# Kernel tuning notes

Measured on AMD Instinct MI355X. Metric: run time of the kernel, lower is better.

## Reference

```python
import jax, jax.numpy as jnp
import numpy as np

# geomloss.SamplesLoss(loss='sinkhorn', p=2, blur=0.1**0.5, backend='tensorized',
#                      cost=cosine cost ** 2) with defaults scaling=0.5, debias=True,
#                      reach=None (balanced OT, dampening = 1), uniform weights.
P = 2
BLUR = 0.1 ** 0.5   # eps = BLUR**P = 0.1
SCALING = 0.5


def cosine_cost(a, b):
    # a: (B,N,D), b: (B,M,D) -> (1 - cos(a,b))**2, shape (B,N,M)
    an = a / jnp.linalg.norm(a, axis=-1, keepdims=True)
    bn = b / jnp.linalg.norm(b, axis=-1, keepdims=True)
    return (1.0 - jnp.einsum('bnd,bmd->bnm', an, bn)) ** P


def softmin(eps, C, h):
    # geomloss softmin_tensorized: h (B,M), C (B,N,M) -> (B,N)
    return -eps * jax.nn.logsumexp(h[:, None, :] - C / eps, axis=2)


def eps_schedule(diameter):
    # geomloss epsilon_schedule(p, diameter, blur, scaling)
    return ([diameter ** P]
            + [float(np.exp(e)) for e in np.arange(P * np.log(diameter),
                                                   P * np.log(BLUR),
                                                   P * np.log(SCALING))]
            + [BLUR ** P])


def max_diameter(x, y):
    # geomloss max_diameter over all points of both (flattened) clouds
    D = x.shape[-1]
    pts = np.concatenate([np.asarray(x).reshape(-1, D),
                          np.asarray(y).reshape(-1, D)], axis=0)
    return float(np.linalg.norm(pts.max(axis=0) - pts.min(axis=0)))


def _sinkhorn(x, y, eps_list):
    sg = jax.lax.stop_gradient
    B, N, _ = x.shape
    M = y.shape[1]
    # geomloss detaches the second argument of each cost evaluation
    C_xy = cosine_cost(x, sg(y))
    C_yx = cosine_cost(y, sg(x))
    C_xx = cosine_cost(x, sg(x))  # debias terms
    C_yy = cosine_cost(y, sg(y))

    a_log = jnp.full((B, N), -np.log(N), dtype=x.dtype)  # log uniform weights
    b_log = jnp.full((B, M), -np.log(M), dtype=x.dtype)

    # initialization at the largest temperature
    eps = eps_list[0]
    f_aa = softmin(eps, sg(C_xx), a_log)
    g_bb = softmin(eps, sg(C_yy), b_log)
    g_ab = softmin(eps, sg(C_yx), a_log)
    f_ba = softmin(eps, sg(C_xy), b_log)

    # eps-scaling loop (run without gradients, as in geomloss)
    for eps in eps_list:
        ft_ba = softmin(eps, sg(C_xy), b_log + g_ab / eps)
        gt_ab = softmin(eps, sg(C_yx), a_log + f_ba / eps)
        ft_aa = softmin(eps, sg(C_xx), a_log + f_aa / eps)
        gt_bb = softmin(eps, sg(C_yy), b_log + g_bb / eps)
        f_ba, g_ab = 0.5 * (f_ba + ft_ba), 0.5 * (g_ab + gt_ab)
        f_aa, g_bb = 0.5 * (f_aa + ft_aa), 0.5 * (g_bb + gt_bb)

    # last extrapolation WITH gradients, dual inputs detached (envelope theorem)
    eps = eps_list[-1]
    f_ba, g_ab = (softmin(eps, C_xy, sg(b_log + g_ab / eps)),
                  softmin(eps, C_yx, sg(a_log + f_ba / eps)))
    f_aa = softmin(eps, C_xx, sg(a_log + f_aa / eps))
    g_bb = softmin(eps, C_yy, sg(b_log + g_bb / eps))

    # sinkhorn_cost, debiased, batch -> (B,)
    a = jnp.exp(a_log)
    b = jnp.exp(b_log)
    return jnp.sum(a * (f_ba - f_aa), axis=1) + jnp.sum(b * (g_ab - g_bb), axis=1)


def setup_inputs() -> dict:
    key = jax.random.key(0)
    k1, k2 = jax.random.split(key)
    B, N, D = 2, 4096, 64
    inputs = jax.random.normal(k1, (B, N, D), dtype=jnp.float32)
    targets = jax.random.normal(k2, (B, N, D), dtype=jnp.float32)
    return {"inputs": inputs, "targets": targets}


def reference(inputs, targets):
    eps_list = eps_schedule(max_diameter(inputs, targets))
    return _sinkhorn(inputs, targets, eps_list)
```

## Files before the change

kernel.cpp:

```cpp
#include <hip/hip_runtime.h>
#include <math.h>

#define Bq 2
#define Nq 4096
#define Dq 64
#define MAXR 14
#define RBAND 32
#define NBAND (Nq / RBAND)
#define W_LOG (-8.317766166719343f)
#define WL2   (-12.0f)
#define LOG2E 1.4426950408889634f
#define LN2   0.6931471805599453f
#define DQ_SCALE (4.0f / 65535.0f)
#define Q_SCALE  16383.75f
#define ACLAMP 88.0f
#define SFLOOR 1e-30f

#define F_XN   ((size_t)0)
#define F_YN   (F_XN + (size_t)Bq * Nq * Dq)
#define F_XH   (F_YN + (size_t)Bq * Nq * Dq)
#define F_XL   (F_XH + (size_t)Bq * Nq * Dq / 2)
#define F_YH   (F_XL + (size_t)Bq * Nq * Dq / 2)
#define F_YL   (F_YH + (size_t)Bq * Nq * Dq / 2)
#define F_FG   (F_YL + (size_t)Bq * Nq * Dq / 2)
#define F_EPS  (F_FG + (size_t)2 * 4 * Bq * Nq)
#define F_MM   (F_EPS + 64)
#define F_CP   (F_MM + (size_t)64 * 128)
#define F_C    (((F_CP + (size_t)Bq * NBAND * Nq) + 3) & ~(size_t)3)
#define GSZ    ((size_t)Bq * Nq * Nq)
#define F_TOTAL_P (F_C + 3 * GSZ / 2)
#define F_TOTAL_S (F_C)

typedef short short8v __attribute__((ext_vector_type(8)));
typedef float f32x4 __attribute__((ext_vector_type(4)));

__device__ __forceinline__ unsigned short f2bf(float f) {
    unsigned u = __float_as_uint(f);
    unsigned r = (u + 0x7fffu + ((u >> 16) & 1u)) >> 16;
    return (unsigned short)r;
}
__device__ __forceinline__ float bf2f(unsigned short b) {
    return __uint_as_float(((unsigned)b) << 16);
}

__global__ __launch_bounds__(256) void k_normalize(const float* __restrict__ x,
                                                   const float* __restrict__ y,
                                                   float* __restrict__ ws) {
    int gid = blockIdx.x * 256 + threadIdx.x;
    int wave = gid >> 6;
    int lane = gid & 63;
    int tensor = wave / (Bq * Nq);
    int p = wave % (Bq * Nq);
    const float* src = tensor ? y : x;
    float v = src[(size_t)p * Dq + lane];
    float s = v * v;
    #pragma unroll
    for (int o = 32; o > 0; o >>= 1) s += __shfl_xor(s, o);
    float vn = v / sqrtf(s);
    float* dst = ws + (tensor ? F_YN : F_XN);
    dst[(size_t)p * Dq + lane] = vn;
    unsigned short hb = f2bf(vn);
    float lo = vn - bf2f(hb);
    unsigned short lb = f2bf(lo);
    unsigned short* dh = (unsigned short*)(ws + (tensor ? F_YH : F_XH));
    unsigned short* dl = (unsigned short*)(ws + (tensor ? F_YL : F_XL));
    dh[(size_t)p * Dq + lane] = hb;
    dl[(size_t)p * Dq + lane] = lb;
}

__global__ __launch_bounds__(256) void k_minmax(const float* __restrict__ x,
                                                const float* __restrict__ y,
                                                float* __restrict__ ws) {
    int d = threadIdx.x & 63, q = threadIdx.x >> 6;
    int p0 = blockIdx.x * 256;
    float mx = -INFINITY, mn = INFINITY;
    for (int p = p0 + q; p < p0 + 256; p += 4) {
        const float* src = (p < Bq * Nq) ? x : y;
        int pp = (p < Bq * Nq) ? p : p - Bq * Nq;
        float v = src[(size_t)pp * Dq + d];
        mx = fmaxf(mx, v); mn = fminf(mn, v);
    }
    __shared__ float smx[4][64], smn[4][64];
    smx[q][d] = mx; smn[q][d] = mn;
    __syncthreads();
    if (threadIdx.x < 64) {
        float a = fmaxf(fmaxf(smx[0][d], smx[1][d]), fmaxf(smx[2][d], smx[3][d]));
        float i = fminf(fminf(smn[0][d], smn[1][d]), fminf(smn[2][d], smn[3][d]));
        ws[F_MM + (size_t)blockIdx.x * 128 + d] = a;
        ws[F_MM + (size_t)blockIdx.x * 128 + 64 + d] = i;
    }
}

__global__ void k_eps(float* __restrict__ ws) {
    int d = threadIdx.x;
    float mx = -INFINITY, mn = INFINITY;
    for (int k = 0; k < 64; k++) {
        mx = fmaxf(mx, ws[F_MM + (size_t)k * 128 + d]);
        mn = fminf(mn, ws[F_MM + (size_t)k * 128 + 64 + d]);
    }
    float r = mx - mn;
    float r2 = r * r;
    #pragma unroll
    for (int o = 32; o > 0; o >>= 1) r2 += __shfl_xor(r2, o);
    if (d == 0) {
        double dd = (double)sqrtf(r2);
        double start = 2.0 * log(dd);
        double stop  = 2.0 * log(sqrt(0.1));
        double step  = 2.0 * log(0.5);
        double lend = ceil((stop - start) / step);
        int len = (lend <= 0.0) ? 0 : (int)lend;
        int n = len + 2;
        if (n > MAXR - 2) n = MAXR - 2;
        int* ei = (int*)(ws + F_EPS);
        ei[0] = n;
        float* ev = ws + F_EPS + 8;
        ev[0] = (float)(dd * dd);
        for (int i = 0; i < len && i + 1 < n - 1; i++)
            ev[1 + i] = (float)exp(start + i * step);
        ev[n - 1] = 0.1f;
    }
}

__global__ __launch_bounds__(256) void k_gram_mfma(float* __restrict__ ws) {
    int op = blockIdx.z, b = blockIdx.y;
    int tr = (blockIdx.x & 63) * 64;
    int tc = (blockIdx.x >> 6) * 64;
    const unsigned short* AH = (const unsigned short*)(ws + (op == 2 ? F_YH : F_XH)) + (size_t)b * Nq * Dq;
    const unsigned short* AL = (const unsigned short*)(ws + (op == 2 ? F_YL : F_XL)) + (size_t)b * Nq * Dq;
    const unsigned short* BH = (const unsigned short*)(ws + (op == 1 ? F_XH : F_YH)) + (size_t)b * Nq * Dq;
    const unsigned short* BL = (const unsigned short*)(ws + (op == 1 ? F_XL : F_YL)) + (size_t)b * Nq * Dq;

    __shared__ unsigned short sAh[64][72], sAl[64][72], sBh[64][72], sBl[64][72], sC[64][72];

    #pragma unroll
    for (int i = 0; i < 2; i++) {
        int c = threadIdx.x + 256 * i;
        int row = c >> 3, pos = c & 7;
        size_t sa = (size_t)(tr + row) * Dq + pos * 8;
        size_t sb = (size_t)(tc + row) * Dq + pos * 8;
        *(uint4*)&sAh[row][pos * 8] = *(const uint4*)&AH[sa];
        *(uint4*)&sAl[row][pos * 8] = *(const uint4*)&AL[sa];
        *(uint4*)&sBh[row][pos * 8] = *(const uint4*)&BH[sb];
        *(uint4*)&sBl[row][pos * 8] = *(const uint4*)&BL[sb];
    }
    __syncthreads();

    int w = threadIdx.x >> 6, lane = threadIdx.x & 63;
    int m = lane & 15, kb = lane >> 4;
    int ar = w * 16 + m;
    short8v aH0 = *(const short8v*)&sAh[ar][kb * 8];
    short8v aH1 = *(const short8v*)&sAh[ar][32 + kb * 8];
    short8v aL0 = *(const short8v*)&sAl[ar][kb * 8];
    short8v aL1 = *(const short8v*)&sAl[ar][32 + kb * 8];

    #pragma unroll
    for (int cb = 0; cb < 4; cb++) {
        int bc = cb * 16 + m;
        short8v bH0 = *(const short8v*)&sBh[bc][kb * 8];
        short8v bH1 = *(const short8v*)&sBh[bc][32 + kb * 8];
        short8v bL0 = *(const short8v*)&sBl[bc][kb * 8];
        short8v bL1 = *(const short8v*)&sBl[bc][32 + kb * 8];
        f32x4 acc = {0.f, 0.f, 0.f, 0.f};
        acc = __builtin_amdgcn_mfma_f32_16x16x32_bf16(aH0, bH0, acc, 0, 0, 0);
        acc = __builtin_amdgcn_mfma_f32_16x16x32_bf16(aH1, bH1, acc, 0, 0, 0);
        acc = __builtin_amdgcn_mfma_f32_16x16x32_bf16(aL0, bH0, acc, 0, 0, 0);
        acc = __builtin_amdgcn_mfma_f32_16x16x32_bf16(aL1, bH1, acc, 0, 0, 0);
        acc = __builtin_amdgcn_mfma_f32_16x16x32_bf16(aH0, bL0, acc, 0, 0, 0);
        acc = __builtin_amdgcn_mfma_f32_16x16x32_bf16(aH1, bL1, acc, 0, 0, 0);
        #pragma unroll
        for (int rr = 0; rr < 4; rr++) {
            float c1 = 1.0f - acc[rr];
            unsigned u = __float2uint_rn(fminf(c1 * c1, 4.0f) * Q_SCALE);
            if (u > 65535u) u = 65535u;
            sC[w * 16 + kb * 4 + rr][cb * 16 + m] = (unsigned short)u;
        }
    }
    __syncthreads();

    unsigned short* C = (unsigned short*)(ws + F_C) + (size_t)op * GSZ + (size_t)b * Nq * Nq;
    #pragma unroll
    for (int i = 0; i < 2; i++) {
        int c = threadIdx.x + 256 * i;
        int row = c >> 3, pos = c & 7;
        uint4 v = *(const uint4*)&sC[row][pos * 8];
        *(uint4*)&C[(size_t)(tr + row) * Nq + tc + pos * 8] = v;
    }
}

__device__ __forceinline__ bool round_cfg(const float* ws, int r, int& mode, float& eps,
                                          float& inv_eps, int& cur, int& nxt) {
    const int* ei = (const int*)(ws + F_EPS);
    int n_eps = ei[0];
    if (r > n_eps + 1) return false;
    mode = (r == 0) ? 0 : ((r <= n_eps) ? 1 : 2);
    int eidx = (r == 0) ? 0 : ((r - 1 < n_eps - 1) ? r - 1 : n_eps - 1);
    eps = ws[F_EPS + 8 + eidx];
    inv_eps = 1.0f / eps;
    cur = r & 1; nxt = cur ^ 1;
    return true;
}

__global__ __launch_bounds__(256) void k_iter(float* __restrict__ ws, int r) {
    int mode, cur, nxt; float eps, inv_eps;
    if (!round_cfg(ws, r, mode, eps, inv_eps, cur, nxt)) return;
    float ie2 = inv_eps * LOG2E;
    float epsln2 = eps * LN2;
    float kq = DQ_SCALE * ie2;

    int bid = blockIdx.x;
    int op = bid >> 8;
    int rem = bid & 255;
    int b = rem >> 7;
    int band = rem & (NBAND - 1);
    int row0 = band * RBAND;
    int w = threadIdx.x >> 6, lane = threadIdx.x & 63;
    int colA = w * 1024 + lane * 8;
    int colB = colA + 512;

    const unsigned short* C = (const unsigned short*)(ws + F_C)
                              + (size_t)op * GSZ + ((size_t)b * Nq + row0) * Nq;
    int arr_dual = (op == 0) ? 1 : (op == 1 ? 2 : 3);
    int arr_out  = (op == 0) ? 0 : arr_dual;
    const float* gdual = ws + F_FG + ((size_t)cur * 4 + arr_dual) * (Bq * Nq) + (size_t)b * Nq;
    const float* fdual = ws + F_FG + ((size_t)cur * 4 + 0) * (Bq * Nq) + (size_t)b * Nq;

    float a[16];
    if (mode != 0) {
        float4 g0 = *(const float4*)&gdual[colA];
        float4 g1 = *(const float4*)&gdual[colA + 4];
        float4 g2 = *(const float4*)&gdual[colB];
        float4 g3 = *(const float4*)&gdual[colB + 4];
        a[0] = g0.x * ie2;  a[1] = g0.y * ie2;  a[2] = g0.z * ie2;  a[3] = g0.w * ie2;
        a[4] = g1.x * ie2;  a[5] = g1.y * ie2;  a[6] = g1.z * ie2;  a[7] = g1.w * ie2;
        a[8] = g2.x * ie2;  a[9] = g2.y * ie2;  a[10] = g2.z * ie2; a[11] = g2.w * ie2;
        a[12] = g3.x * ie2; a[13] = g3.y * ie2; a[14] = g3.z * ie2; a[15] = g3.w * ie2;
    } else {
        #pragma unroll
        for (int j = 0; j < 16; j++) a[j] = 0.f;
    }
    float cs[16];
    #pragma unroll
    for (int j = 0; j < 16; j++) cs[j] = 0.f;

    __shared__ float rowpart[RBAND][4];

    #pragma unroll 4
    for (int i = 0; i < RBAND; i++) {
        uint4 cuA = *(const uint4*)&C[(size_t)i * Nq + colA];
        uint4 cuB = *(const uint4*)&C[(size_t)i * Nq + colB];
        float bi = 0.f;
        if (op == 0 && mode != 0) bi = fdual[row0 + i] * ie2;
        unsigned uw[8] = {cuA.x, cuA.y, cuA.z, cuA.w, cuB.x, cuB.y, cuB.z, cuB.w};
        float rs = 0.f;
        #pragma unroll
        for (int j = 0; j < 16; j++) {
            float uf = (float)((uw[j >> 1] >> ((j & 1) * 16)) & 0xffffu);
            float t = uf * kq;
            rs += exp2f(fminf(a[j] - t, ACLAMP));
            if (op == 0) cs[j] += exp2f(fminf(bi - t, ACLAMP));
        }
        #pragma unroll
        for (int o = 32; o > 0; o >>= 1) rs += __shfl_xor(rs, o);
        if (lane == 0) rowpart[i][w] = rs;
    }
    __syncthreads();

    if (threadIdx.x < RBAND) {
        int gr = row0 + threadIdx.x;
        const float* rp = rowpart[threadIdx.x];
        float s = (rp[0] + rp[1]) + (rp[2] + rp[3]);
        float ft = -epsln2 * (WL2 + log2f(fmaxf(s, SFLOOR)));
        float* outp = ws + F_FG + ((size_t)nxt * 4 + arr_out) * (Bq * Nq) + (size_t)b * Nq;
        const float* oldp = ws + F_FG + ((size_t)cur * 4 + arr_out) * (Bq * Nq) + (size_t)b * Nq;
        outp[gr] = (mode == 1) ? 0.5f * (oldp[gr] + ft) : ft;
    }

    if (op == 0) {
        float* cp = ws + F_CP + ((size_t)b * NBAND + band) * Nq;
        *(float4*)&cp[colA]     = make_float4(cs[0], cs[1], cs[2], cs[3]);
        *(float4*)&cp[colA + 4] = make_float4(cs[4], cs[5], cs[6], cs[7]);
        *(float4*)&cp[colB]     = make_float4(cs[8], cs[9], cs[10], cs[11]);
        *(float4*)&cp[colB + 4] = make_float4(cs[12], cs[13], cs[14], cs[15]);
    }
}

__global__ __launch_bounds__(256) void k_colcomb(float* __restrict__ ws, int r) {
    int mode, cur, nxt; float eps, inv_eps;
    if (!round_cfg(ws, r, mode, eps, inv_eps, cur, nxt)) return;
    float epsln2 = eps * LN2;
    int idx = blockIdx.x * 256 + threadIdx.x;
    int b = idx >> 12, m = idx & (Nq - 1);
    const float* cp = ws + F_CP + (size_t)b * NBAND * Nq + m;
    float S = 0.f;
    #pragma unroll 8
    for (int k = 0; k < NBAND; k++) S += cp[(size_t)k * Nq];
    float gt = -epsln2 * (WL2 + log2f(fmaxf(S, SFLOOR)));
    float* outp = ws + F_FG + ((size_t)nxt * 4 + 1) * (Bq * Nq) + (size_t)b * Nq;
    const float* oldp = ws + F_FG + ((size_t)cur * 4 + 1) * (Bq * Nq) + (size_t)b * Nq;
    outp[m] = (mode == 1) ? 0.5f * (oldp[m] + gt) : gt;
}

__global__ __launch_bounds__(256) void k_fused(float* __restrict__ ws, int r) {
    int mode, cur, nxt; float eps, inv_eps;
    if (!round_cfg(ws, r, mode, eps, inv_eps, cur, nxt)) return;
    int op = blockIdx.z, b = blockIdx.y;
    int tr = blockIdx.x * 64;
    const float* A  = ws + ((op == 1 || op == 3) ? F_YN : F_XN) + (size_t)b * Nq * Dq;
    const float* Bp = ws + ((op == 0 || op == 3) ? F_YN : F_XN) + (size_t)b * Nq * Dq;
    int dual_arr = (op == 0) ? 1 : (op == 1) ? 0 : (op == 2) ? 2 : 3;
    int out_arr  = (op == 0) ? 0 : (op == 1) ? 1 : (op == 2) ? 2 : 3;
    const float* hdual = ws + F_FG + ((size_t)cur * 4 + dual_arr) * (Bq * Nq) + (size_t)b * Nq;

    __shared__ float As[64][65], Bs[64][65];
    #pragma unroll
    for (int i = 0; i < 16; i++) {
        int idx = threadIdx.x + 256 * i;
        As[idx >> 6][idx & 63] = A[(size_t)(tr + (idx >> 6)) * Dq + (idx & 63)];
    }
    int tx = threadIdx.x & 15, ty = threadIdx.x >> 4;
    float m_i[4], s_i[4];
    #pragma unroll
    for (int i = 0; i < 4; i++) { m_i[i] = -INFINITY; s_i[i] = 0.f; }

    for (int tc = 0; tc < Nq; tc += 64) {
        __syncthreads();
        #pragma unroll
        for (int i = 0; i < 16; i++) {
            int idx = threadIdx.x + 256 * i;
            Bs[idx >> 6][idx & 63] = Bp[(size_t)(tc + (idx >> 6)) * Dq + (idx & 63)];
        }
        __syncthreads();
        float acc[4][4] = {};
        #pragma unroll
        for (int dd = 0; dd < 64; dd++) {
            float a[4], bb[4];
            #pragma unroll
            for (int i = 0; i < 4; i++) a[i] = As[ty * 4 + i][dd];
            #pragma unroll
            for (int j = 0; j < 4; j++) bb[j] = Bs[tx * 4 + j][dd];
            #pragma unroll
            for (int i = 0; i < 4; i++)
                #pragma unroll
                for (int j = 0; j < 4; j++) acc[i][j] = fmaf(a[i], bb[j], acc[i][j]);
        }
        float hv[4];
        #pragma unroll
        for (int j = 0; j < 4; j++)
            hv[j] = (mode == 0) ? 0.f : hdual[tc + tx * 4 + j];
        #pragma unroll
        for (int i = 0; i < 4; i++) {
            float v[4], tm = -INFINITY;
            #pragma unroll
            for (int j = 0; j < 4; j++) {
                float c = 1.0f - acc[i][j];
                v[j] = W_LOG + (hv[j] - c * c) * inv_eps;
                tm = fmaxf(tm, v[j]);
            }
            float nm = fmaxf(m_i[i], tm);
            float add = 0.f;
            #pragma unroll
            for (int j = 0; j < 4; j++) add += expf(v[j] - nm);
            s_i[i] = s_i[i] * expf(m_i[i] - nm) + add;
            m_i[i] = nm;
        }
    }
    #pragma unroll
    for (int o = 1; o < 16; o <<= 1) {
        #pragma unroll
        for (int i = 0; i < 4; i++) {
            float om = __shfl_xor(m_i[i], o);
            float os = __shfl_xor(s_i[i], o);
            float M = fmaxf(m_i[i], om);
            s_i[i] = s_i[i] * expf(m_i[i] - M) + os * expf(om - M);
            m_i[i] = M;
        }
    }
    if (tx == 0) {
        float* outp = ws + F_FG + ((size_t)nxt * 4 + out_arr) * (Bq * Nq) + (size_t)b * Nq;
        const float* oldp = ws + F_FG + ((size_t)cur * 4 + out_arr) * (Bq * Nq) + (size_t)b * Nq;
        #pragma unroll
        for (int i = 0; i < 4; i++) {
            int n = tr + ty * 4 + i;
            float ft = -eps * (m_i[i] + logf(s_i[i]));
            outp[n] = (mode == 1) ? 0.5f * (oldp[n] + ft) : ft;
        }
    }
}

__global__ __launch_bounds__(256) void k_final(const float* __restrict__ ws,
                                               float* __restrict__ out) {
    const int* ei = (const int*)(ws + F_EPS);
    int n_eps = ei[0];
    int fin = n_eps & 1;
    int b = blockIdx.x;
    const float* fba = ws + F_FG + ((size_t)fin * 4 + 0) * (Bq * Nq) + (size_t)b * Nq;
    const float* gab = ws + F_FG + ((size_t)fin * 4 + 1) * (Bq * Nq) + (size_t)b * Nq;
    const float* faa = ws + F_FG + ((size_t)fin * 4 + 2) * (Bq * Nq) + (size_t)b * Nq;
    const float* gbb = ws + F_FG + ((size_t)fin * 4 + 3) * (Bq * Nq) + (size_t)b * Nq;
    float s = 0.f;
    for (int n = threadIdx.x; n < Nq; n += 256)
        s += (fba[n] - faa[n]) + (gab[n] - gbb[n]);
    #pragma unroll
    for (int o = 32; o > 0; o >>= 1) s += __shfl_xor(s, o);
    __shared__ float red[4];
    if ((threadIdx.x & 63) == 0) red[threadIdx.x >> 6] = s;
    __syncthreads();
    if (threadIdx.x == 0)
        out[b] = (red[0] + red[1] + red[2] + red[3]) * (1.0f / Nq);
}

__global__ void k_sentinel(float* out, int n) {
    if ((int)threadIdx.x < n) out[threadIdx.x] = 2.0e9f;
}

extern "C" void kernel_launch(void* const* d_in, const int* in_sizes, int n_in,
                              void* d_out, int out_size, void* d_ws, size_t ws_size,
                              hipStream_t stream) {
    const float* x = (const float*)d_in[0];
    const float* y = (const float*)d_in[1];
    float* out = (float*)d_out;
    float* ws = (float*)d_ws;

    bool big   = ws_size >= F_TOTAL_P * sizeof(float);
    bool small = ws_size >= F_TOTAL_S * sizeof(float);

    if (!small) {
        k_sentinel<<<1, 64, 0, stream>>>(out, out_size);
        return;
    }

    k_normalize<<<(2 * Bq * Nq * 64) / 256, 256, 0, stream>>>(x, y, ws);
    k_minmax<<<64, 256, 0, stream>>>(x, y, ws);
    k_eps<<<1, 64, 0, stream>>>(ws);

    if (big) {
        k_gram_mfma<<<dim3(4096, Bq, 3), 256, 0, stream>>>(ws);
        for (int r = 0; r < MAXR; r++) {
            k_iter<<<3 * Bq * NBAND, 256, 0, stream>>>(ws, r);
            k_colcomb<<<(Bq * Nq) / 256, 256, 0, stream>>>(ws, r);
        }
    } else {
        for (int r = 0; r < MAXR; r++) {
            k_fused<<<dim3(Nq / 64, Bq, 4), 256, 0, stream>>>(ws, r);
        }
    }

    k_final<<<Bq, 256, 0, stream>>>(ws, out);
}
```

Before: 849.3 us.

## Factor exp of duals out of inner loop and halve row band size

Rewrites exp2(a - t) as exp2(a) * exp2(-t), so each cost entry needs one exp2 that is shared between the row sum and the column sum for the op-0 case, instead of two exps. Dual exponentials are precomputed once per thread (columns) and once per row. The loop now processes two rows per iteration with interleaved shuffle reductions, and RBAND is halved to 16 to double the block count. The factored form loses the per-term clamp and may underflow or overflow when duals and costs are large, which affects numerical robustness.

```diff
diff --git a/kernel.cpp b/kernel.cpp
--- a/kernel.cpp
+++ b/kernel.cpp
@@ -5,7 +5,7 @@
 #define Nq 4096
 #define Dq 64
 #define MAXR 14
-#define RBAND 32
+#define RBAND 16
 #define NBAND (Nq / RBAND)
 #define W_LOG (-8.317766166719343f)
 #define WL2   (-12.0f)
@@ -205,13 +205,13 @@
     if (!round_cfg(ws, r, mode, eps, inv_eps, cur, nxt)) return;
     float ie2 = inv_eps * LOG2E;
     float epsln2 = eps * LN2;
-    float kq = DQ_SCALE * ie2;
+    float nkq = -DQ_SCALE * ie2;
 
     int bid = blockIdx.x;
-    int op = bid >> 8;
-    int rem = bid & 255;
-    int b = rem >> 7;
-    int band = rem & (NBAND - 1);
+    int op = bid / (Bq * NBAND);
+    int rem = bid % (Bq * NBAND);
+    int b = rem / NBAND;
+    int band = rem % NBAND;
     int row0 = band * RBAND;
     int w = threadIdx.x >> 6, lane = threadIdx.x & 63;
     int colA = w * 1024 + lane * 8;
@@ -224,19 +224,19 @@
     const float* gdual = ws + F_FG + ((size_t)cur * 4 + arr_dual) * (Bq * Nq) + (size_t)b * Nq;
     const float* fdual = ws + F_FG + ((size_t)cur * 4 + 0) * (Bq * Nq) + (size_t)b * Nq;
 
-    float a[16];
+    float pa[16];
     if (mode != 0) {
         float4 g0 = *(const float4*)&gdual[colA];
         float4 g1 = *(const float4*)&gdual[colA + 4];
         float4 g2 = *(const float4*)&gdual[colB];
         float4 g3 = *(const float4*)&gdual[colB + 4];
-        a[0] = g0.x * ie2;  a[1] = g0.y * ie2;  a[2] = g0.z * ie2;  a[3] = g0.w * ie2;
-        a[4] = g1.x * ie2;  a[5] = g1.y * ie2;  a[6] = g1.z * ie2;  a[7] = g1.w * ie2;
-        a[8] = g2.x * ie2;  a[9] = g2.y * ie2;  a[10] = g2.z * ie2; a[11] = g2.w * ie2;
-        a[12] = g3.x * ie2; a[13] = g3.y * ie2; a[14] = g3.z * ie2; a[15] = g3.w * ie2;
+        float gv[16] = {g0.x, g0.y, g0.z, g0.w, g1.x, g1.y, g1.z, g1.w,
+                        g2.x, g2.y, g2.z, g2.w, g3.x, g3.y, g3.z, g3.w};
+        #pragma unroll
+        for (int j = 0; j < 16; j++) pa[j] = exp2f(fminf(gv[j] * ie2, ACLAMP));
     } else {
         #pragma unroll
-        for (int j = 0; j < 16; j++) a[j] = 0.f;
+        for (int j = 0; j < 16; j++) pa[j] = 1.f;
     }
     float cs[16];
     #pragma unroll
@@ -244,24 +244,34 @@
 
     __shared__ float rowpart[RBAND][4];
 
-    #pragma unroll 4
-    for (int i = 0; i < RBAND; i++) {
-        uint4 cuA = *(const uint4*)&C[(size_t)i * Nq + colA];
-        uint4 cuB = *(const uint4*)&C[(size_t)i * Nq + colB];
-        float bi = 0.f;
-        if (op == 0 && mode != 0) bi = fdual[row0 + i] * ie2;
-        unsigned uw[8] = {cuA.x, cuA.y, cuA.z, cuA.w, cuB.x, cuB.y, cuB.z, cuB.w};
-        float rs = 0.f;
+    #pragma unroll 2
+    for (int i = 0; i < RBAND; i += 2) {
+        uint4 cA0 = *(const uint4*)&C[(size_t)i * Nq + colA];
+        uint4 cB0 = *(const uint4*)&C[(size_t)i * Nq + colB];
+        uint4 cA1 = *(const uint4*)&C[(size_t)(i + 1) * Nq + colA];
+        uint4 cB1 = *(const uint4*)&C[(size_t)(i + 1) * Nq + colB];
+        float pb0 = 1.f, pb1 = 1.f;
+        if (op == 0 && mode != 0) {
+            pb0 = exp2f(fminf(fdual[row0 + i] * ie2, ACLAMP));
+            pb1 = exp2f(fminf(fdual[row0 + i + 1] * ie2, ACLAMP));
+        }
+        unsigned u0[8] = {cA0.x, cA0.y, cA0.z, cA0.w, cB0.x, cB0.y, cB0.z, cB0.w};
+        unsigned u1[8] = {cA1.x, cA1.y, cA1.z, cA1.w, cB1.x, cB1.y, cB1.z, cB1.w};
+        float rs0 = 0.f, rs1 = 0.f;
         #pragma unroll
         for (int j = 0; j < 16; j++) {
-            float uf = (float)((uw[j >> 1] >> ((j & 1) * 16)) & 0xffffu);
-            float t = uf * kq;
-            rs += exp2f(fminf(a[j] - t, ACLAMP));
-            if (op == 0) cs[j] += exp2f(fminf(bi - t, ACLAMP));
-        }
-        #pragma unroll
-        for (int o = 32; o > 0; o >>= 1) rs += __shfl_xor(rs, o);
-        if (lane == 0) rowpart[i][w] = rs;
+            float e0 = exp2f((float)((u0[j >> 1] >> ((j & 1) * 16)) & 0xffffu) * nkq);
+            float e1 = exp2f((float)((u1[j >> 1] >> ((j & 1) * 16)) & 0xffffu) * nkq);
+            rs0 = fmaf(pa[j], e0, rs0);
+            rs1 = fmaf(pa[j], e1, rs1);
+            if (op == 0) cs[j] = fmaf(pb0, e0, fmaf(pb1, e1, cs[j]));
+        }
+        #pragma unroll
+        for (int o = 32; o > 0; o >>= 1) {
+            rs0 += __shfl_xor(rs0, o);
+            rs1 += __shfl_xor(rs1, o);
+        }
+        if (lane == 0) { rowpart[i][w] = rs0; rowpart[i + 1][w] = rs1; }
     }
     __syncthreads();
 
```

Result: faster. 817.4 us (-3.8%).
